# Optimization experiments

Measured on AMD Instinct MI355X. Metric: run time of the kernel, lower is better.

The kernel has to match this reference:

```python
import jax, jax.numpy as jnp
import numpy as np

NX, NY, NZ = 432, 496, 1
VX, VY, VZ = 0.16, 0.16, 4.0
XOFF = VX / 2 + 0.0
YOFF = VY / 2 + (-39.68)
ZOFF = VZ / 2 + (-3.0)
GRID = NZ * NX * NY
P, NPT, B = 100000, 32, 8
EPS = 1e-3


def setup_inputs() -> dict:
    key = jax.random.key(0)
    k1, k2, k3, k4 = jax.random.split(key, 4)
    voxels = jax.random.normal(k1, (P, NPT, 4), dtype=jnp.float32)
    num_points = jax.random.randint(k2, (P,), 1, NPT + 1, dtype=jnp.int32)
    b = jax.random.randint(k3, (P,), 0, B, dtype=jnp.int32)
    # unique BEV cells (17 coprime with GRID, P < GRID) -> deterministic scatter
    cell = (jnp.arange(P, dtype=jnp.int32) * 17) % GRID
    y = cell // NX
    x = cell % NX
    coords = jnp.stack([b, jnp.zeros_like(b), y, x], axis=1)  # [P,4] (b,z,y,x)
    W = jax.random.normal(k4, (64, 10), dtype=jnp.float32) * 0.1
    gamma = jnp.ones((64,), dtype=jnp.float32)
    beta = jnp.zeros((64,), dtype=jnp.float32)
    return {"voxels": voxels, "num_points": num_points, "coords": coords,
            "W": W, "gamma": gamma, "beta": beta}


def reference(voxels, num_points, coords, W, gamma, beta):
    cf = coords.astype(voxels.dtype)
    npf = num_points.astype(voxels.dtype)
    # cluster feature: offset from pillar mean
    points_mean = voxels[:, :, :3].sum(axis=1, keepdims=True) / npf[:, None, None]
    f_cluster = voxels[:, :, :3] - points_mean
    # center feature: offset from voxel center
    cx = cf[:, 3, None] * VX + XOFF
    cy = cf[:, 2, None] * VY + YOFF
    cz = cf[:, 1, None] * VZ + ZOFF
    f_center = jnp.stack([voxels[:, :, 0] - cx,
                          voxels[:, :, 1] - cy,
                          voxels[:, :, 2] - cz], axis=-1)
    feat = jnp.concatenate([voxels, f_cluster, f_center], axis=-1)  # [P,N,10]
    mask = (jnp.arange(NPT, dtype=jnp.int32)[None, :] < num_points[:, None])
    feat = feat * mask.astype(feat.dtype)[:, :, None]
    # linear(10->64, no bias) + BatchNorm1d (batch stats, biased var) + relu
    x = jnp.einsum('pnf,cf->pnc', feat, W)  # [P,N,64]
    mean = x.mean(axis=(0, 1))
    var = ((x - mean) ** 2).mean(axis=(0, 1))
    x = (x - mean) * jax.lax.rsqrt(var + EPS) * gamma + beta
    x = jax.nn.relu(x)
    pillars = x.max(axis=1)  # [P,64]
    idx = coords[:, 1] + coords[:, 2] * NX + coords[:, 3]
    bev = jnp.zeros((B, GRID, 64), dtype=pillars.dtype)
    bev = bev.at[coords[:, 0], idx].set(pillars)
    bev = jnp.transpose(bev, (0, 2, 1))  # [B,64,GRID]
    return bev.reshape(B, 64 * NZ, NY, NX)
```

## Files before the change

### kernel.cpp

```cpp
#include <hip/hip_runtime.h>

typedef unsigned short u16;

#define NXg 432
#define NYg 496
#define GRIDg (NXg*NYg)
#define NPTg 32
#define Bg 8
#define CHg 64
#define NSLOT 32

__device__ __forceinline__ float bf2f(u16 u){
    union { unsigned int i; float f; } x; x.i = ((unsigned int)u) << 16; return x.f;
}
__device__ __forceinline__ u16 f2bf(float f){
    union { float f; unsigned int i; } x; x.f = f;
    unsigned int i = x.i + 0x7FFFu + ((x.i >> 16) & 1u);
    return (u16)(i >> 16);
}
__device__ __forceinline__ bool is_bf16(const void* gamma){
    return ((*(const unsigned*)gamma) & 0xFFFFu) != 0u;
}
__device__ __forceinline__ float rdlane(float v, int k){
    return __int_as_float(__builtin_amdgcn_readlane(__float_as_int(v), k));
}

__global__ __launch_bounds__(256) void pfe_init(int* __restrict__ map, float* __restrict__ chsum){
    int t = blockIdx.x*256 + threadIdx.x;
    ((int4*)map)[t] = make_int4(-1,-1,-1,-1);
    if (t < (NSLOT*128)/4) ((float4*)chsum)[t] = make_float4(0.f,0.f,0.f,0.f);
}

__global__ __launch_bounds__(256) void pfe_pillar(
    const void* __restrict__ vox, const int* __restrict__ nump,
    const int* __restrict__ coords, const void* __restrict__ Wv,
    const void* __restrict__ gv,
    u16* __restrict__ pv, int* __restrict__ map, float* __restrict__ chsum,
    int P, int nwaves)
{
    const bool isbf = is_bf16(gv);
    int lane = threadIdx.x & 63;
    int wid  = (blockIdx.x*256 + threadIdx.x) >> 6;
    int n    = lane & 31;

    float w4,w5,w6,w7,w8,w9, wp0,wp1,wp2,wp3;
    bool gsel;
    {
        float w[10];
#pragma unroll
        for (int j=0;j<10;j++)
            w[j] = isbf ? bf2f(((const u16*)Wv)[lane*10 + j]) : ((const float*)Wv)[lane*10 + j];
        wp0 = w[0]+w[4]+w[7];
        wp1 = w[1]+w[5]+w[8];
        wp2 = w[2]+w[6]+w[9];
        wp3 = w[3];
        w4=w[4]; w5=w[5]; w6=w[6]; w7=w[7]; w8=w[8]; w9=w[9];
        float g = isbf ? bf2f(((const u16*)gv)[lane]) : ((const float*)gv)[lane];
        gsel = (g >= 0.f);
    }

    float sx = 0.f, sx2 = 0.f;

    for (int p = wid; p < P; p += nwaves) {
        int np = nump[p];
        int4 cc = *(const int4*)(coords + 4*p);
        float4 pt;
        if (isbf){
            ushort4 raw = *(const ushort4*)((const u16*)vox + ((size_t)p*NPTg + n)*4);
            pt = make_float4(bf2f(raw.x), bf2f(raw.y), bf2f(raw.z), bf2f(raw.w));
        } else {
            pt = *(const float4*)((const float*)vox + ((size_t)p*NPTg + n)*4);
        }

        float s0 = pt.x, s1 = pt.y, s2 = pt.z;
#pragma unroll
        for (int m = 1; m < 64; m <<= 1){
            s0 += __shfl_xor(s0, m, 64);
            s1 += __shfl_xor(s1, m, 64);
            s2 += __shfl_xor(s2, m, 64);
        }
        float inv = 0.5f / (float)np;
        float m0 = s0*inv, m1 = s1*inv, m2 = s2*inv;
        float ccx = (float)cc.w * 0.16f + 0.08f;
        float ccy = (float)cc.z * 0.16f + (0.08f - 39.68f);
        float ccz = (float)cc.y * 4.0f  + (2.0f - 3.0f);
        float d = -(m0*w4 + m1*w5 + m2*w6 + ccx*w7 + ccy*w8 + ccz*w9);

        float qmx = -3e38f, qmn = 3e38f, sq = 0.f, sq2 = 0.f;
        int k = 0;
        for (; k + 4 <= np; k += 4){
#pragma unroll
            for (int u = 0; u < 4; u++){
                float ax = rdlane(pt.x, k+u);
                float ay = rdlane(pt.y, k+u);
                float az = rdlane(pt.z, k+u);
                float aw = rdlane(pt.w, k+u);
                float q = fmaf(ax, wp0, fmaf(ay, wp1, fmaf(az, wp2, aw*wp3)));
                qmx = fmaxf(qmx, q);
                qmn = fminf(qmn, q);
                sq += q;
                sq2 = fmaf(q, q, sq2);
            }
        }
        for (; k < np; k++){
            float ax = rdlane(pt.x, k);
            float ay = rdlane(pt.y, k);
            float az = rdlane(pt.z, k);
            float aw = rdlane(pt.w, k);
            float q = fmaf(ax, wp0, fmaf(ay, wp1, fmaf(az, wp2, aw*wp3)));
            qmx = fmaxf(qmx, q);
            qmn = fminf(qmn, q);
            sq += q;
            sq2 = fmaf(q, q, sq2);
        }

        float npf = (float)np;
        sx  += sq + npf*d;
        sx2 += sq2 + d*(2.f*sq + npf*d);

        float fmx = qmx + d, fmn = qmn + d;
        if (np < NPTg){ fmx = fmaxf(fmx, 0.f); fmn = fminf(fmn, 0.f); }
        pv[(size_t)p*CHg + lane] = f2bf(gsel ? fmx : fmn);
        if (lane == 0) map[cc.x*GRIDg + cc.z*NXg + cc.w] = p;
    }

    float* slot = chsum + (blockIdx.x & (NSLOT-1))*128;
    atomicAdd(slot + lane, sx);
    atomicAdd(slot + 64 + lane, sx2);
}

__global__ __launch_bounds__(64) void pfe_stats(
    const float* __restrict__ chsum,
    const void* __restrict__ gv, const void* __restrict__ bv,
    float* __restrict__ sb, int P)
{
    const bool isbf = is_bf16(gv);
    int t = threadIdx.x;
    float S = 0.f, S2 = 0.f;
    for (int sl = 0; sl < NSLOT; sl++){
        S  += chsum[sl*128 + t];
        S2 += chsum[sl*128 + 64 + t];
    }
    float cnt = (float)P * (float)NPTg;
    float mean = S / cnt;
    float var  = S2 / cnt - mean*mean;
    float g  = isbf ? bf2f(((const u16*)gv)[t]) : ((const float*)gv)[t];
    float be = isbf ? bf2f(((const u16*)bv)[t]) : ((const float*)bv)[t];
    float sc = g * rsqrtf(var + 1e-3f);
    sb[t] = sc; sb[64 + t] = be - mean*sc;
}

__global__ __launch_bounds__(192) void pfe_gather(
    const int* __restrict__ map, const u16* __restrict__ pv,
    const float* __restrict__ sb, const void* __restrict__ gv,
    void* __restrict__ out)
{
    const bool isbf = is_bf16(gv);
    int b  = blockIdx.z;
    int c0 = blockIdx.y * 32;
    int px = blockIdx.x*384 + threadIdx.x*2;
    int2 m2 = *(const int2*)(map + (size_t)b*GRIDg + px);
    bool v0 = m2.x >= 0, v1 = m2.y >= 0;
    int p0 = v0 ? m2.x : 0;
    int p1 = v1 ? m2.y : 0;

    uint4 R0[4], R1[4];
    const uint4* r0p = (const uint4*)(pv + (size_t)p0*CHg + c0);
    const uint4* r1p = (const uint4*)(pv + (size_t)p1*CHg + c0);
#pragma unroll
    for (int i = 0; i < 4; i++){ R0[i] = r0p[i]; R1[i] = r1p[i]; }

    unsigned mask01 = (v0 ? 0x0000FFFFu : 0u) | (v1 ? 0xFFFF0000u : 0u);

#pragma unroll
    for (int j = 0; j < 32; j++){
        float sc = sb[c0 + j];
        float bi = sb[64 + c0 + j];
        unsigned d0 = ((const unsigned*)R0)[j >> 1];
        unsigned d1 = ((const unsigned*)R1)[j >> 1];
        float x0 = __uint_as_float((j & 1) ? (d0 & 0xFFFF0000u) : (d0 << 16));
        float x1 = __uint_as_float((j & 1) ? (d1 & 0xFFFF0000u) : (d1 << 16));
        float r0 = fmaxf(fmaf(sc, x0, bi), 0.f);
        float r1 = fmaxf(fmaf(sc, x1, bi), 0.f);
        size_t obase = ((size_t)(b*CHg + c0 + j))*GRIDg + px;
        if (isbf){
            unsigned pk = ((unsigned)f2bf(r0) | ((unsigned)f2bf(r1) << 16)) & mask01;
            *(unsigned*)((u16*)out + obase) = pk;
        } else {
            float2 o;
            o.x = v0 ? r0 : 0.f;
            o.y = v1 ? r1 : 0.f;
            *(float2*)((float*)out + obase) = o;
        }
    }
}

extern "C" void kernel_launch(void* const* d_in, const int* in_sizes, int n_in,
                              void* d_out, int out_size, void* d_ws, size_t ws_size,
                              hipStream_t stream)
{
    const void* vox   = d_in[0];
    const int* nump   = (const int*)d_in[1];
    const int* coords = (const int*)d_in[2];
    const void* Wv    = d_in[3];
    const void* gv    = d_in[4];
    const void* bv    = d_in[5];
    int P = in_sizes[1];

    float* chsum = (float*)d_ws;
    float* sb    = (float*)((char*)d_ws + 16384);
    u16*   pv    = (u16*)((char*)d_ws + 32768);
    int*   map   = (int*)((char*)pv + (size_t)P*CHg*2);

    int initThreads = (Bg*GRIDg)/4;
    pfe_init<<<initThreads/256, 256, 0, stream>>>(map, chsum);

    int blocks1 = 2048;
    pfe_pillar<<<blocks1, 256, 0, stream>>>(vox, nump, coords, Wv, gv, pv, map, chsum, P, blocks1*4);

    pfe_stats<<<1, 64, 0, stream>>>(chsum, gv, bv, sb, P);

    dim3 g3(GRIDg/384, 2, Bg);
    pfe_gather<<<g3, 192, 0, stream>>>(map, pv, sb, gv, d_out);
}
```

Baseline: 538.4 us.

## Widen gather to four pixels per thread and split pillar reduction accumulators

The gather kernel now has each thread handle four adjacent BEV pixels, using int4 map loads and float4/uint2 output stores, in 64-thread blocks. The aim is to cut store instruction count and improve write coalescing for the large output. The pillar kernel makes the pillar index wave-uniform with readfirstlane so loads can use scalar paths. It shortens the shuffle reduction to 32 lanes and drops the 0.5 factor, and it splits the max/min/sum accumulators four ways to break dependency chains. Tiny 64-thread blocks and the higher register count per thread may hurt occupancy.

```diff
diff --git a/kernel.cpp b/kernel.cpp
--- a/kernel.cpp
+++ b/kernel.cpp
@@ -62,31 +62,35 @@
     float sx = 0.f, sx2 = 0.f;
 
     for (int p = wid; p < P; p += nwaves) {
-        int np = nump[p];
-        int4 cc = *(const int4*)(coords + 4*p);
+        int ps = __builtin_amdgcn_readfirstlane(p);
+        int np = nump[ps];
+        int4 cc = *(const int4*)(coords + 4*ps);
         float4 pt;
         if (isbf){
-            ushort4 raw = *(const ushort4*)((const u16*)vox + ((size_t)p*NPTg + n)*4);
+            ushort4 raw = *(const ushort4*)((const u16*)vox + ((size_t)ps*NPTg + n)*4);
             pt = make_float4(bf2f(raw.x), bf2f(raw.y), bf2f(raw.z), bf2f(raw.w));
         } else {
-            pt = *(const float4*)((const float*)vox + ((size_t)p*NPTg + n)*4);
+            pt = *(const float4*)((const float*)vox + ((size_t)ps*NPTg + n)*4);
         }
 
         float s0 = pt.x, s1 = pt.y, s2 = pt.z;
 #pragma unroll
-        for (int m = 1; m < 64; m <<= 1){
+        for (int m = 1; m < 32; m <<= 1){
             s0 += __shfl_xor(s0, m, 64);
             s1 += __shfl_xor(s1, m, 64);
             s2 += __shfl_xor(s2, m, 64);
         }
-        float inv = 0.5f / (float)np;
+        float inv = 1.0f / (float)np;
         float m0 = s0*inv, m1 = s1*inv, m2 = s2*inv;
         float ccx = (float)cc.w * 0.16f + 0.08f;
         float ccy = (float)cc.z * 0.16f + (0.08f - 39.68f);
         float ccz = (float)cc.y * 4.0f  + (2.0f - 3.0f);
         float d = -(m0*w4 + m1*w5 + m2*w6 + ccx*w7 + ccy*w8 + ccz*w9);
 
-        float qmx = -3e38f, qmn = 3e38f, sq = 0.f, sq2 = 0.f;
+        float qmxa[4] = {-3e38f,-3e38f,-3e38f,-3e38f};
+        float qmna[4] = { 3e38f, 3e38f, 3e38f, 3e38f};
+        float sqa[4]  = {0.f,0.f,0.f,0.f};
+        float sq2a[4] = {0.f,0.f,0.f,0.f};
         int k = 0;
         for (; k + 4 <= np; k += 4){
 #pragma unroll
@@ -96,23 +100,27 @@
                 float az = rdlane(pt.z, k+u);
                 float aw = rdlane(pt.w, k+u);
                 float q = fmaf(ax, wp0, fmaf(ay, wp1, fmaf(az, wp2, aw*wp3)));
-                qmx = fmaxf(qmx, q);
-                qmn = fminf(qmn, q);
-                sq += q;
-                sq2 = fmaf(q, q, sq2);
+                qmxa[u] = fmaxf(qmxa[u], q);
+                qmna[u] = fminf(qmna[u], q);
+                sqa[u] += q;
+                sq2a[u] = fmaf(q, q, sq2a[u]);
             }
         }
-        for (; k < np; k++){
+        for (int u = 0; k < np; k++, u++){
             float ax = rdlane(pt.x, k);
             float ay = rdlane(pt.y, k);
             float az = rdlane(pt.z, k);
             float aw = rdlane(pt.w, k);
             float q = fmaf(ax, wp0, fmaf(ay, wp1, fmaf(az, wp2, aw*wp3)));
-            qmx = fmaxf(qmx, q);
-            qmn = fminf(qmn, q);
-            sq += q;
-            sq2 = fmaf(q, q, sq2);
-        }
+            qmxa[u] = fmaxf(qmxa[u], q);
+            qmna[u] = fminf(qmna[u], q);
+            sqa[u] += q;
+            sq2a[u] = fmaf(q, q, sq2a[u]);
+        }
+        float qmx = fmaxf(fmaxf(qmxa[0], qmxa[1]), fmaxf(qmxa[2], qmxa[3]));
+        float qmn = fminf(fminf(qmna[0], qmna[1]), fminf(qmna[2], qmna[3]));
+        float sq  = (sqa[0]  + sqa[1])  + (sqa[2]  + sqa[3]);
+        float sq2 = (sq2a[0] + sq2a[1]) + (sq2a[2] + sq2a[3]);
 
         float npf = (float)np;
         sx  += sq + npf*d;
@@ -120,8 +128,8 @@
 
         float fmx = qmx + d, fmn = qmn + d;
         if (np < NPTg){ fmx = fmaxf(fmx, 0.f); fmn = fminf(fmn, 0.f); }
-        pv[(size_t)p*CHg + lane] = f2bf(gsel ? fmx : fmn);
-        if (lane == 0) map[cc.x*GRIDg + cc.z*NXg + cc.w] = p;
+        pv[(size_t)ps*CHg + lane] = f2bf(gsel ? fmx : fmn);
+        if (lane == 0) map[cc.x*GRIDg + cc.z*NXg + cc.w] = ps;
     }
 
     float* slot = chsum + (blockIdx.x & (NSLOT-1))*128;
@@ -150,7 +158,7 @@
     sb[t] = sc; sb[64 + t] = be - mean*sc;
 }
 
-__global__ __launch_bounds__(192) void pfe_gather(
+__global__ __launch_bounds__(64) void pfe_gather(
     const int* __restrict__ map, const u16* __restrict__ pv,
     const float* __restrict__ sb, const void* __restrict__ gv,
     void* __restrict__ out)
@@ -158,39 +166,39 @@
     const bool isbf = is_bf16(gv);
     int b  = blockIdx.z;
     int c0 = blockIdx.y * 32;
-    int px = blockIdx.x*384 + threadIdx.x*2;
-    int2 m2 = *(const int2*)(map + (size_t)b*GRIDg + px);
-    bool v0 = m2.x >= 0, v1 = m2.y >= 0;
-    int p0 = v0 ? m2.x : 0;
-    int p1 = v1 ? m2.y : 0;
-
-    uint4 R0[4], R1[4];
-    const uint4* r0p = (const uint4*)(pv + (size_t)p0*CHg + c0);
-    const uint4* r1p = (const uint4*)(pv + (size_t)p1*CHg + c0);
-#pragma unroll
-    for (int i = 0; i < 4; i++){ R0[i] = r0p[i]; R1[i] = r1p[i]; }
-
-    unsigned mask01 = (v0 ? 0x0000FFFFu : 0u) | (v1 ? 0xFFFF0000u : 0u);
+    int px = blockIdx.x*256 + threadIdx.x*4;
+    int4 m4 = *(const int4*)(map + (size_t)b*GRIDg + px);
+    int pidx[4] = {m4.x, m4.y, m4.z, m4.w};
+    bool val[4];
+    uint4 R[4][4];
+#pragma unroll
+    for (int i = 0; i < 4; i++){
+        val[i] = pidx[i] >= 0;
+        int p = val[i] ? pidx[i] : 0;
+        const uint4* rp = (const uint4*)(pv + (size_t)p*CHg + c0);
+        R[i][0] = rp[0]; R[i][1] = rp[1]; R[i][2] = rp[2]; R[i][3] = rp[3];
+    }
 
 #pragma unroll
     for (int j = 0; j < 32; j++){
         float sc = sb[c0 + j];
         float bi = sb[64 + c0 + j];
-        unsigned d0 = ((const unsigned*)R0)[j >> 1];
-        unsigned d1 = ((const unsigned*)R1)[j >> 1];
-        float x0 = __uint_as_float((j & 1) ? (d0 & 0xFFFF0000u) : (d0 << 16));
-        float x1 = __uint_as_float((j & 1) ? (d1 & 0xFFFF0000u) : (d1 << 16));
-        float r0 = fmaxf(fmaf(sc, x0, bi), 0.f);
-        float r1 = fmaxf(fmaf(sc, x1, bi), 0.f);
+        float r[4];
+#pragma unroll
+        for (int i = 0; i < 4; i++){
+            unsigned dw = ((const unsigned*)R[i])[j >> 1];
+            float x = __uint_as_float((j & 1) ? (dw & 0xFFFF0000u) : (dw << 16));
+            r[i] = val[i] ? fmaxf(fmaf(sc, x, bi), 0.f) : 0.f;
+        }
         size_t obase = ((size_t)(b*CHg + c0 + j))*GRIDg + px;
         if (isbf){
-            unsigned pk = ((unsigned)f2bf(r0) | ((unsigned)f2bf(r1) << 16)) & mask01;
-            *(unsigned*)((u16*)out + obase) = pk;
+            uint2 pk;
+            pk.x = (unsigned)f2bf(r[0]) | ((unsigned)f2bf(r[1]) << 16);
+            pk.y = (unsigned)f2bf(r[2]) | ((unsigned)f2bf(r[3]) << 16);
+            *(uint2*)((u16*)out + obase) = pk;
         } else {
-            float2 o;
-            o.x = v0 ? r0 : 0.f;
-            o.y = v1 ? r1 : 0.f;
-            *(float2*)((float*)out + obase) = o;
+            float4 o; o.x = r[0]; o.y = r[1]; o.z = r[2]; o.w = r[3];
+            *(float4*)((float*)out + obase) = o;
         }
     }
 }
@@ -220,6 +228,6 @@
 
     pfe_stats<<<1, 64, 0, stream>>>(chsum, gv, bv, sb, P);
 
-    dim3 g3(GRIDg/384, 2, Bg);
-    pfe_gather<<<g3, 192, 0, stream>>>(map, pv, sb, gv, d_out);
-}
+    dim3 g3(GRIDg/256, 2, Bg);
+    pfe_gather<<<g3, 64, 0, stream>>>(map, pv, sb, gv, d_out);
+}
```

Result: slower. 555.9 us (+3.3%).
